# Optimization experiments

Measured on AMD Instinct MI355X. Metric: run time of the kernel, lower is better.

The kernel has to match this reference:

```python
import jax, jax.numpy as jnp
import numpy as np

B, T, E, H = 8, 2048, 1024, 64

def setup_inputs() -> dict:
    key = jax.random.key(0)
    kx, kk, kq, kv = jax.random.split(key, 4)
    x = jax.random.normal(kx, (B, T, E), dtype=jnp.float32)
    # nn.Linear(n_embd, head_size, bias=False): weight (H, E); store as (E, H) for x @ W
    Wk = jax.random.normal(kk, (E, H), dtype=jnp.float32) / np.sqrt(E)
    Wq = jax.random.normal(kq, (E, H), dtype=jnp.float32) / np.sqrt(E)
    Wv = jax.random.normal(kv, (E, H), dtype=jnp.float32) / np.sqrt(E)
    return {"x": x, "Wk": Wk, "Wq": Wq, "Wv": Wv}

def reference(x, Wk, Wq, Wv):
    # Single causal self-attention head (dropout in eval mode = identity).
    Bd, Td, Ed = x.shape
    k = x @ Wk  # [B,T,H]
    q = x @ Wq  # [B,T,H]
    v = x @ Wv  # [B,T,H]
    scale = jnp.asarray(64, x.dtype) ** -0.5  # hardcoded E2=64 in source
    wei = jnp.einsum('bth,bsh->bts', q, k) * scale  # [B,T,T]
    causal = jnp.tril(jnp.ones((Td, Td), dtype=bool))
    wei = jnp.where(causal, wei, -jnp.inf)
    wei = jax.nn.softmax(wei, axis=-1)
    out = jnp.einsum('bts,bsh->bth', wei, v)  # [B,T,H]
    return out
```

## Files before the change

kernel.cpp:

```cpp
#include <hip/hip_runtime.h>
#include <hip/hip_bf16.h>


typedef float f32x4 __attribute__((ext_vector_type(4)));
typedef float f32x16 __attribute__((ext_vector_type(16)));
typedef short bf16x8 __attribute__((ext_vector_type(8)));
typedef short bf16x4 __attribute__((ext_vector_type(4)));
typedef unsigned u32x2 __attribute__((ext_vector_type(2)));

#define MFMA16 __builtin_amdgcn_mfma_f32_16x16x32_bf16
#define MFMA32 __builtin_amdgcn_mfma_f32_32x32x16_bf16

__device__ __forceinline__ short f2bf(float f) {
    union { float f; unsigned u; } c; c.f = f;
    unsigned u = c.u;
    return (short)((u + 0x7FFFu + ((u >> 16) & 1u)) >> 16);
}

__device__ __forceinline__ unsigned cvt_pk_bf16(float lo, float hi) {
    unsigned r;
    asm("v_cvt_pk_bf16_f32 %0, %1, %2" : "=v"(r) : "v"(lo), "v"(hi));
    return r;
}

__global__ __launch_bounds__(256) void prep_w(const float* __restrict__ Wk,
                                              const float* __restrict__ Wq,
                                              const float* __restrict__ Wv,
                                              short* __restrict__ wsT) {
    int idx = blockIdx.x * 256 + threadIdx.x;
    int r = idx >> 10;
    int k = idx & 1023;
    int mat = r >> 6, c = r & 63;
    const float* W = (mat == 0) ? Wk : (mat == 1) ? Wq : Wv;
    float v = W[k * 64 + c];
    if (mat == 1) v *= 0.125f * 1.44269504088896f;
    wsT[r * 1024 + k] = f2bf(v);
}

__global__ __launch_bounds__(512, 4) void proj(const float* __restrict__ x,
                                               const short* __restrict__ wsT,
                                               short* __restrict__ kF,
                                               short* __restrict__ qF,
                                               short* __restrict__ vF) {
    __shared__ char ldsraw[2 * 8192 + 2 * 24576];
    int tid = threadIdx.x;
    int w = tid >> 6, lane = tid & 63;
    int wm = w >> 2, wn = w & 3;
    int lr = lane & 15, lg = lane >> 4;
    int t0 = blockIdx.x * 32;

    f32x4 acc[3] = {};

    auto stage = [&](int kt, int buf) {
        int k0 = kt * 64;
        {
            int G = tid;
            int row = G >> 4, p = G & 15;
            int g = p ^ (row & 15);
            const float* gp = x + (size_t)(t0 + row) * 1024 + k0 + g * 4;
            unsigned base = (unsigned)(buf * 8192 + w * 1024);
            __builtin_amdgcn_global_load_lds(
                (const __attribute__((address_space(1))) void*)gp,
                (__attribute__((address_space(3))) void*)(ldsraw + base), 16, 0, 0);
        }
#pragma unroll
        for (int s = 0; s < 3; ++s) {
            int G = s * 512 + tid;
            int row = G >> 3, p = G & 7;
            int g = p ^ (row & 7);
            const short* gp = wsT + (size_t)row * 1024 + k0 + g * 8;
            unsigned base = (unsigned)(16384 + buf * 24576 + s * 8192 + w * 1024);
            __builtin_amdgcn_global_load_lds(
                (const __attribute__((address_space(1))) void*)gp,
                (__attribute__((address_space(3))) void*)(ldsraw + base), 16, 0, 0);
        }
    };

    int arow = wm * 16 + lr;

    stage(0, 0);
    __syncthreads();

    for (int kt = 0; kt < 16; ++kt) {
        int cur = kt & 1;
        if (kt < 15) stage(kt + 1, cur ^ 1);

        const char* xb = ldsraw + cur * 8192 + arow * 256;
        const char* wb = ldsraw + 16384 + cur * 24576;
#pragma unroll
        for (int ks = 0; ks < 2; ++ks) {
            int g0 = ks * 8 + lg * 2;
            f32x4 u0 = *(const f32x4*)(xb + ((g0)     ^ lr) * 16);
            f32x4 u1 = *(const f32x4*)(xb + ((g0 + 1) ^ lr) * 16);
            bf16x8 a;
#pragma unroll
            for (int j = 0; j < 4; ++j) { a[j] = f2bf(u0[j]); a[4 + j] = f2bf(u1[j]); }
            int slot = (ks * 4 + lg) ^ (lr & 7);
#pragma unroll
            for (int nt = 0; nt < 3; ++nt) {
                int brow = wn * 48 + nt * 16 + lr;
                bf16x8 bf = *(const bf16x8*)(wb + brow * 128 + slot * 16);
                acc[nt] = MFMA16(a, bf, acc[nt], 0, 0, 0);
            }
        }
        __syncthreads();
    }

    int tg = t0 + wm * 16 + lg * 4;
    int b = tg >> 11;
    int s = (tg & 2047) >> 5;
    int w32b = tg & 31;
#pragma unroll
    for (int nt = 0; nt < 3; ++nt) {
        int col0 = wn * 48 + nt * 16;
        int mat = col0 >> 6;
        int h = (col0 & 63) + lr;
        if (mat == 2) {
            int ht = h >> 5;
            int c = w32b >> 4;
            int hi2 = (lg >> 1) & 1;
            int jb = (lg & 1) * 4;
            int lanep = hi2 * 32 + (h & 31);
            bf16x4 pk;
#pragma unroll
            for (int r = 0; r < 4; ++r) pk[r] = f2bf(acc[nt][r]);
            size_t idx = (((((size_t)b * 64 + s) * 2 + ht) * 2 + c) * 64 + lanep) * 8 + jb;
            *(bf16x4*)(vF + idx) = pk;
        } else {
            short* dst = mat ? qF : kF;
            int c = h >> 4, hi2 = (h >> 3) & 1, j = h & 7;
            size_t base = ((((size_t)b * 64 + s) * 4 + c) * 64 + hi2 * 32) * 8 + j;
#pragma unroll
            for (int r = 0; r < 4; ++r)
                dst[base + (size_t)(w32b + r) * 8] = f2bf(acc[nt][r]);
        }
    }
}

__global__ __launch_bounds__(512, 4) void attn(const short* __restrict__ kF,
                                               const short* __restrict__ qF,
                                               const short* __restrict__ vF,
                                               float* __restrict__ out) {
    int bid = blockIdx.x;
    int b = bid & 7;
    int i = bid >> 3;
    int ti = (i & 1) ? (63 - (i >> 1)) : (i >> 1);
    int t0 = ti * 32;

    int w = threadIdx.x >> 6;
    int lane = threadIdx.x & 63;
    int q = lane & 31, hi = lane >> 5;

    __shared__ float lacc[8][32][65];
    __shared__ float lm[8][32], ll[8][32];

    const short* qp = qF + ((size_t)(b * 64 + ti)) * 2048 + lane * 8;
    bf16x8 qf0 = *(const bf16x8*)(qp);
    bf16x8 qf1 = *(const bf16x8*)(qp + 512);
    bf16x8 qf2 = *(const bf16x8*)(qp + 1024);
    bf16x8 qf3 = *(const bf16x8*)(qp + 1536);

    const short* kb_b = kF + (size_t)b * 64 * 2048 + lane * 8;
    const short* vb_b = vF + (size_t)b * 64 * 2048 + lane * 8;

    f32x16 acc0 = {}, acc1 = {};
    float m_s = -1e30f, l_s = 0.f;

    int nblk = ti + 1;
    for (int blk = w; blk < nblk; blk += 8) {
        const short* kp = kb_b + (size_t)blk * 2048;
        bf16x8 kf0 = *(const bf16x8*)(kp);
        bf16x8 kf1 = *(const bf16x8*)(kp + 512);
        bf16x8 kf2 = *(const bf16x8*)(kp + 1024);
        bf16x8 kf3 = *(const bf16x8*)(kp + 1536);

        f32x16 S = {};
        S = MFMA32(kf0, qf0, S, 0, 0, 0);
        S = MFMA32(kf1, qf1, S, 0, 0, 0);
        S = MFMA32(kf2, qf2, S, 0, 0, 0);
        S = MFMA32(kf3, qf3, S, 0, 0, 0);

        const short* vp = vb_b + (size_t)blk * 2048;
        bf16x8 vf00 = *(const bf16x8*)(vp);
        bf16x8 vf01 = *(const bf16x8*)(vp + 512);
        bf16x8 vf10 = *(const bf16x8*)(vp + 1024);
        bf16x8 vf11 = *(const bf16x8*)(vp + 1536);

        if (blk == ti) {
#pragma unroll
            for (int r = 0; r < 16; ++r) {
                int row = (r & 3) + 8 * (r >> 2) + 4 * hi;
                if (row > q) S[r] = -1e30f;
            }
        }

        float a0 = fmaxf(S[0], S[1]),   a1 = fmaxf(S[2], S[3]);
        float a2 = fmaxf(S[4], S[5]),   a3 = fmaxf(S[6], S[7]);
        float a4 = fmaxf(S[8], S[9]),   a5 = fmaxf(S[10], S[11]);
        float a6 = fmaxf(S[12], S[13]), a7 = fmaxf(S[14], S[15]);
        a0 = fmaxf(a0, a1); a2 = fmaxf(a2, a3);
        a4 = fmaxf(a4, a5); a6 = fmaxf(a6, a7);
        a0 = fmaxf(a0, a2); a4 = fmaxf(a4, a6);
        float tm = fmaxf(a0, a4);
        tm = fmaxf(tm, __shfl_xor(tm, 32));

        bool skip = __all(tm <= m_s);
        float mn = skip ? m_s : fmaxf(m_s, tm);

#pragma unroll
        for (int r = 0; r < 16; ++r) S[r] = exp2f(S[r] - mn);
        float b0 = (S[0] + S[1]) + (S[2] + S[3]);
        float b1 = (S[4] + S[5]) + (S[6] + S[7]);
        float b2 = (S[8] + S[9]) + (S[10] + S[11]);
        float b3 = (S[12] + S[13]) + (S[14] + S[15]);
        float rs = (b0 + b1) + (b2 + b3);
        rs += __shfl_xor(rs, 32);

        if (skip) {
            l_s += rs;
        } else {
            float fr = exp2f(m_s - mn);
            l_s = l_s * fr + rs;
            m_s = mn;
#pragma unroll
            for (int r = 0; r < 16; ++r) { acc0[r] *= fr; acc1[r] *= fr; }
        }

        unsigned pk0 = cvt_pk_bf16(S[0],  S[1]);
        unsigned pk1 = cvt_pk_bf16(S[2],  S[3]);
        unsigned pk2 = cvt_pk_bf16(S[4],  S[5]);
        unsigned pk3 = cvt_pk_bf16(S[6],  S[7]);
        unsigned pk4 = cvt_pk_bf16(S[8],  S[9]);
        unsigned pk5 = cvt_pk_bf16(S[10], S[11]);
        unsigned pk6 = cvt_pk_bf16(S[12], S[13]);
        unsigned pk7 = cvt_pk_bf16(S[14], S[15]);
        u32x2 s02 = __builtin_amdgcn_permlane32_swap(pk0, pk2, false, false);
        u32x2 s13 = __builtin_amdgcn_permlane32_swap(pk1, pk3, false, false);
        u32x2 s46 = __builtin_amdgcn_permlane32_swap(pk4, pk6, false, false);
        u32x2 s57 = __builtin_amdgcn_permlane32_swap(pk5, pk7, false, false);
        union { bf16x8 v; unsigned u[4]; } f0, f1;
        f0.u[0] = s02.x; f0.u[1] = s13.x; f0.u[2] = s02.y; f0.u[3] = s13.y;
        f1.u[0] = s46.x; f1.u[1] = s57.x; f1.u[2] = s46.y; f1.u[3] = s57.y;

        acc0 = MFMA32(vf00, f0.v, acc0, 0, 0, 0);
        acc0 = MFMA32(vf01, f1.v, acc0, 0, 0, 0);
        acc1 = MFMA32(vf10, f0.v, acc1, 0, 0, 0);
        acc1 = MFMA32(vf11, f1.v, acc1, 0, 0, 0);
    }

    if (hi == 0) { lm[w][q] = m_s; ll[w][q] = l_s; }
#pragma unroll
    for (int r = 0; r < 16; ++r) {
        int row = (r & 3) + 8 * (r >> 2) + 4 * hi;
        lacc[w][q][row]      = acc0[r];
        lacc[w][q][32 + row] = acc1[r];
    }
    __syncthreads();

    int tid = threadIdx.x;
#pragma unroll
    for (int e = 0; e < 4; ++e) {
        int elem = e * 512 + tid;
        int row = elem >> 6, col = elem & 63;
        float ms = lm[0][row];
#pragma unroll
        for (int j = 1; j < 8; ++j) ms = fmaxf(ms, lm[j][row]);
        float lsum = 0.f, asum = 0.f;
#pragma unroll
        for (int j = 0; j < 8; ++j) {
            float sj = exp2f(lm[j][row] - ms);
            lsum += ll[j][row] * sj;
            asum += lacc[j][row][col] * sj;
        }
        out[(size_t)(b * 2048 + t0 + row) * 64 + col] = asum / lsum;
    }
}

extern "C" void kernel_launch(void* const* d_in, const int* in_sizes, int n_in,
                              void* d_out, int out_size, void* d_ws, size_t ws_size,
                              hipStream_t stream) {
    (void)in_sizes; (void)n_in; (void)out_size; (void)ws_size;
    const float* x  = (const float*)d_in[0];
    const float* Wk = (const float*)d_in[1];
    const float* Wq = (const float*)d_in[2];
    const float* Wv = (const float*)d_in[3];
    float* out = (float*)d_out;

    char* ws = (char*)d_ws;
    short* wsT = (short*)(ws);
    short* kF  = (short*)(ws + (1u << 20));
    short* qF  = (short*)(ws + (3u << 20));
    short* vF  = (short*)(ws + (5u << 20));

    prep_w<<<768, 256, 0, stream>>>(Wk, Wq, Wv, wsT);
    proj  <<<512, 512, 0, stream>>>(x, wsT, kF, qF, vF);
    attn  <<<512, 512, 0, stream>>>(kF, qF, vF, out);
}
```

Measured before the change: 43.48 us.

## Pair causal tiles per block, prefetch next K/V, and relax rescale threshold

Each attention block now processes two query tiles (pj and 63-pj) in turn, so every block gets an equal causal workload, and the grid is halved to 256 blocks. The inner loop double-buffers K/V register fragments, loading the next block's tiles before computing the current one to hide global load latency. The online-softmax rescale is now skipped unless the new max exceeds the running max by more than 11.5, which cuts rescale work but lets exponentials grow up to about 2^11.5 before renormalisation. Dropping the occupancy hint in launch bounds and prefetching into extra registers may lower occupancy.

Result: faster. 42.05 us (-3.3%).

```diff
diff --git a/kernel.cpp b/kernel.cpp
--- a/kernel.cpp
+++ b/kernel.cpp
@@ -137,142 +137,162 @@
     }
 }
 
-__global__ __launch_bounds__(512, 4) void attn(const short* __restrict__ kF,
-                                               const short* __restrict__ qF,
-                                               const short* __restrict__ vF,
-                                               float* __restrict__ out) {
+__global__ __launch_bounds__(512) void attn(const short* __restrict__ kF,
+                                            const short* __restrict__ qF,
+                                            const short* __restrict__ vF,
+                                            float* __restrict__ out) {
     int bid = blockIdx.x;
     int b = bid & 7;
-    int i = bid >> 3;
-    int ti = (i & 1) ? (63 - (i >> 1)) : (i >> 1);
-    int t0 = ti * 32;
+    int pj = bid >> 3;
 
     int w = threadIdx.x >> 6;
     int lane = threadIdx.x & 63;
     int q = lane & 31, hi = lane >> 5;
+    int tid = threadIdx.x;
 
     __shared__ float lacc[8][32][65];
     __shared__ float lm[8][32], ll[8][32];
 
-    const short* qp = qF + ((size_t)(b * 64 + ti)) * 2048 + lane * 8;
-    bf16x8 qf0 = *(const bf16x8*)(qp);
-    bf16x8 qf1 = *(const bf16x8*)(qp + 512);
-    bf16x8 qf2 = *(const bf16x8*)(qp + 1024);
-    bf16x8 qf3 = *(const bf16x8*)(qp + 1536);
-
     const short* kb_b = kF + (size_t)b * 64 * 2048 + lane * 8;
     const short* vb_b = vF + (size_t)b * 64 * 2048 + lane * 8;
 
-    f32x16 acc0 = {}, acc1 = {};
-    float m_s = -1e30f, l_s = 0.f;
-
-    int nblk = ti + 1;
-    for (int blk = w; blk < nblk; blk += 8) {
-        const short* kp = kb_b + (size_t)blk * 2048;
-        bf16x8 kf0 = *(const bf16x8*)(kp);
-        bf16x8 kf1 = *(const bf16x8*)(kp + 512);
-        bf16x8 kf2 = *(const bf16x8*)(kp + 1024);
-        bf16x8 kf3 = *(const bf16x8*)(kp + 1536);
-
-        f32x16 S = {};
-        S = MFMA32(kf0, qf0, S, 0, 0, 0);
-        S = MFMA32(kf1, qf1, S, 0, 0, 0);
-        S = MFMA32(kf2, qf2, S, 0, 0, 0);
-        S = MFMA32(kf3, qf3, S, 0, 0, 0);
-
-        const short* vp = vb_b + (size_t)blk * 2048;
-        bf16x8 vf00 = *(const bf16x8*)(vp);
-        bf16x8 vf01 = *(const bf16x8*)(vp + 512);
-        bf16x8 vf10 = *(const bf16x8*)(vp + 1024);
-        bf16x8 vf11 = *(const bf16x8*)(vp + 1536);
-
-        if (blk == ti) {
-#pragma unroll
-            for (int r = 0; r < 16; ++r) {
-                int row = (r & 3) + 8 * (r >> 2) + 4 * hi;
-                if (row > q) S[r] = -1e30f;
+    for (int sel = 0; sel < 2; ++sel) {
+        int ti = sel ? (63 - pj) : pj;
+        int t0 = ti * 32;
+        int nblk = ti + 1;
+
+        const short* qp = qF + ((size_t)(b * 64 + ti)) * 2048 + lane * 8;
+        bf16x8 qf0 = *(const bf16x8*)(qp);
+        bf16x8 qf1 = *(const bf16x8*)(qp + 512);
+        bf16x8 qf2 = *(const bf16x8*)(qp + 1024);
+        bf16x8 qf3 = *(const bf16x8*)(qp + 1536);
+
+        f32x16 acc0 = {}, acc1 = {};
+        float m_s = -1e30f, l_s = 0.f;
+
+        int fb = (w < nblk) ? w : 0;
+        const short* kp = kb_b + (size_t)fb * 2048;
+        const short* vp = vb_b + (size_t)fb * 2048;
+        bf16x8 kc0 = *(const bf16x8*)(kp);
+        bf16x8 kc1 = *(const bf16x8*)(kp + 512);
+        bf16x8 kc2 = *(const bf16x8*)(kp + 1024);
+        bf16x8 kc3 = *(const bf16x8*)(kp + 1536);
+        bf16x8 vc0 = *(const bf16x8*)(vp);
+        bf16x8 vc1 = *(const bf16x8*)(vp + 512);
+        bf16x8 vc2 = *(const bf16x8*)(vp + 1024);
+        bf16x8 vc3 = *(const bf16x8*)(vp + 1536);
+
+        for (int blk = w; blk < nblk; blk += 8) {
+            int nxt = blk + 8;
+            int ns = (nxt < nblk) ? nxt : blk;
+            const short* kpn = kb_b + (size_t)ns * 2048;
+            const short* vpn = vb_b + (size_t)ns * 2048;
+            bf16x8 kn0 = *(const bf16x8*)(kpn);
+            bf16x8 kn1 = *(const bf16x8*)(kpn + 512);
+            bf16x8 kn2 = *(const bf16x8*)(kpn + 1024);
+            bf16x8 kn3 = *(const bf16x8*)(kpn + 1536);
+            bf16x8 vn0 = *(const bf16x8*)(vpn);
+            bf16x8 vn1 = *(const bf16x8*)(vpn + 512);
+            bf16x8 vn2 = *(const bf16x8*)(vpn + 1024);
+            bf16x8 vn3 = *(const bf16x8*)(vpn + 1536);
+
+            f32x16 S = {};
+            S = MFMA32(kc0, qf0, S, 0, 0, 0);
+            S = MFMA32(kc1, qf1, S, 0, 0, 0);
+            S = MFMA32(kc2, qf2, S, 0, 0, 0);
+            S = MFMA32(kc3, qf3, S, 0, 0, 0);
+
+            if (blk == ti) {
+#pragma unroll
+                for (int r = 0; r < 16; ++r) {
+                    int row = (r & 3) + 8 * (r >> 2) + 4 * hi;
+                    if (row > q) S[r] = -1e30f;
+                }
             }
-        }
-
-        float a0 = fmaxf(S[0], S[1]),   a1 = fmaxf(S[2], S[3]);
-        float a2 = fmaxf(S[4], S[5]),   a3 = fmaxf(S[6], S[7]);
-        float a4 = fmaxf(S[8], S[9]),   a5 = fmaxf(S[10], S[11]);
-        float a6 = fmaxf(S[12], S[13]), a7 = fmaxf(S[14], S[15]);
-        a0 = fmaxf(a0, a1); a2 = fmaxf(a2, a3);
-        a4 = fmaxf(a4, a5); a6 = fmaxf(a6, a7);
-        a0 = fmaxf(a0, a2); a4 = fmaxf(a4, a6);
-        float tm = fmaxf(a0, a4);
-        tm = fmaxf(tm, __shfl_xor(tm, 32));
-
-        bool skip = __all(tm <= m_s);
-        float mn = skip ? m_s : fmaxf(m_s, tm);
-
-#pragma unroll
-        for (int r = 0; r < 16; ++r) S[r] = exp2f(S[r] - mn);
-        float b0 = (S[0] + S[1]) + (S[2] + S[3]);
-        float b1 = (S[4] + S[5]) + (S[6] + S[7]);
-        float b2 = (S[8] + S[9]) + (S[10] + S[11]);
-        float b3 = (S[12] + S[13]) + (S[14] + S[15]);
-        float rs = (b0 + b1) + (b2 + b3);
-        rs += __shfl_xor(rs, 32);
-
-        if (skip) {
-            l_s += rs;
-        } else {
-            float fr = exp2f(m_s - mn);
-            l_s = l_s * fr + rs;
-            m_s = mn;
-#pragma unroll
-            for (int r = 0; r < 16; ++r) { acc0[r] *= fr; acc1[r] *= fr; }
-        }
-
-        unsigned pk0 = cvt_pk_bf16(S[0],  S[1]);
-        unsigned pk1 = cvt_pk_bf16(S[2],  S[3]);
-        unsigned pk2 = cvt_pk_bf16(S[4],  S[5]);
-        unsigned pk3 = cvt_pk_bf16(S[6],  S[7]);
-        unsigned pk4 = cvt_pk_bf16(S[8],  S[9]);
-        unsigned pk5 = cvt_pk_bf16(S[10], S[11]);
-        unsigned pk6 = cvt_pk_bf16(S[12], S[13]);
-        unsigned pk7 = cvt_pk_bf16(S[14], S[15]);
-        u32x2 s02 = __builtin_amdgcn_permlane32_swap(pk0, pk2, false, false);
-        u32x2 s13 = __builtin_amdgcn_permlane32_swap(pk1, pk3, false, false);
-        u32x2 s46 = __builtin_amdgcn_permlane32_swap(pk4, pk6, false, false);
-        u32x2 s57 = __builtin_amdgcn_permlane32_swap(pk5, pk7, false, false);
-        union { bf16x8 v; unsigned u[4]; } f0, f1;
-        f0.u[0] = s02.x; f0.u[1] = s13.x; f0.u[2] = s02.y; f0.u[3] = s13.y;
-        f1.u[0] = s46.x; f1.u[1] = s57.x; f1.u[2] = s46.y; f1.u[3] = s57.y;
-
-        acc0 = MFMA32(vf00, f0.v, acc0, 0, 0, 0);
-        acc0 = MFMA32(vf01, f1.v, acc0, 0, 0, 0);
-        acc1 = MFMA32(vf10, f0.v, acc1, 0, 0, 0);
-        acc1 = MFMA32(vf11, f1.v, acc1, 0, 0, 0);
-    }
-
-    if (hi == 0) { lm[w][q] = m_s; ll[w][q] = l_s; }
-#pragma unroll
-    for (int r = 0; r < 16; ++r) {
-        int row = (r & 3) + 8 * (r >> 2) + 4 * hi;
-        lacc[w][q][row]      = acc0[r];
-        lacc[w][q][32 + row] = acc1[r];
-    }
-    __syncthreads();
-
-    int tid = threadIdx.x;
-#pragma unroll
-    for (int e = 0; e < 4; ++e) {
-        int elem = e * 512 + tid;
-        int row = elem >> 6, col = elem & 63;
-        float ms = lm[0][row];
-#pragma unroll
-        for (int j = 1; j < 8; ++j) ms = fmaxf(ms, lm[j][row]);
-        float lsum = 0.f, asum = 0.f;
-#pragma unroll
-        for (int j = 0; j < 8; ++j) {
-            float sj = exp2f(lm[j][row] - ms);
-            lsum += ll[j][row] * sj;
-            asum += lacc[j][row][col] * sj;
-        }
-        out[(size_t)(b * 2048 + t0 + row) * 64 + col] = asum / lsum;
+
+            float a0 = fmaxf(S[0], S[1]),   a1 = fmaxf(S[2], S[3]);
+            float a2 = fmaxf(S[4], S[5]),   a3 = fmaxf(S[6], S[7]);
+            float a4 = fmaxf(S[8], S[9]),   a5 = fmaxf(S[10], S[11]);
+            float a6 = fmaxf(S[12], S[13]), a7 = fmaxf(S[14], S[15]);
+            a0 = fmaxf(a0, a1); a2 = fmaxf(a2, a3);
+            a4 = fmaxf(a4, a5); a6 = fmaxf(a6, a7);
+            a0 = fmaxf(a0, a2); a4 = fmaxf(a4, a6);
+            float tm = fmaxf(a0, a4);
+            tm = fmaxf(tm, __shfl_xor(tm, 32));
+
+            bool skip = __all(tm <= m_s + 11.5f);
+            float mn = skip ? m_s : fmaxf(m_s, tm);
+
+#pragma unroll
+            for (int r = 0; r < 16; ++r) S[r] = exp2f(S[r] - mn);
+            float b0 = (S[0] + S[1]) + (S[2] + S[3]);
+            float b1 = (S[4] + S[5]) + (S[6] + S[7]);
+            float b2 = (S[8] + S[9]) + (S[10] + S[11]);
+            float b3 = (S[12] + S[13]) + (S[14] + S[15]);
+            float rs = (b0 + b1) + (b2 + b3);
+            rs += __shfl_xor(rs, 32);
+
+            if (skip) {
+                l_s += rs;
+            } else {
+                float fr = exp2f(m_s - mn);
+                l_s = l_s * fr + rs;
+                m_s = mn;
+#pragma unroll
+                for (int r = 0; r < 16; ++r) { acc0[r] *= fr; acc1[r] *= fr; }
+            }
+
+            unsigned pk0 = cvt_pk_bf16(S[0],  S[1]);
+            unsigned pk1 = cvt_pk_bf16(S[2],  S[3]);
+            unsigned pk2 = cvt_pk_bf16(S[4],  S[5]);
+            unsigned pk3 = cvt_pk_bf16(S[6],  S[7]);
+            unsigned pk4 = cvt_pk_bf16(S[8],  S[9]);
+            unsigned pk5 = cvt_pk_bf16(S[10], S[11]);
+            unsigned pk6 = cvt_pk_bf16(S[12], S[13]);
+            unsigned pk7 = cvt_pk_bf16(S[14], S[15]);
+            u32x2 s02 = __builtin_amdgcn_permlane32_swap(pk0, pk2, false, false);
+            u32x2 s13 = __builtin_amdgcn_permlane32_swap(pk1, pk3, false, false);
+            u32x2 s46 = __builtin_amdgcn_permlane32_swap(pk4, pk6, false, false);
+            u32x2 s57 = __builtin_amdgcn_permlane32_swap(pk5, pk7, false, false);
+            union { bf16x8 v; unsigned u[4]; } f0, f1;
+            f0.u[0] = s02.x; f0.u[1] = s13.x; f0.u[2] = s02.y; f0.u[3] = s13.y;
+            f1.u[0] = s46.x; f1.u[1] = s57.x; f1.u[2] = s46.y; f1.u[3] = s57.y;
+
+            acc0 = MFMA32(vc0, f0.v, acc0, 0, 0, 0);
+            acc0 = MFMA32(vc1, f1.v, acc0, 0, 0, 0);
+            acc1 = MFMA32(vc2, f0.v, acc1, 0, 0, 0);
+            acc1 = MFMA32(vc3, f1.v, acc1, 0, 0, 0);
+
+            kc0 = kn0; kc1 = kn1; kc2 = kn2; kc3 = kn3;
+            vc0 = vn0; vc1 = vn1; vc2 = vn2; vc3 = vn3;
+        }
+
+        if (hi == 0) { lm[w][q] = m_s; ll[w][q] = l_s; }
+#pragma unroll
+        for (int r = 0; r < 16; ++r) {
+            int row = (r & 3) + 8 * (r >> 2) + 4 * hi;
+            lacc[w][q][row]      = acc0[r];
+            lacc[w][q][32 + row] = acc1[r];
+        }
+        __syncthreads();
+
+#pragma unroll
+        for (int e = 0; e < 4; ++e) {
+            int elem = e * 512 + tid;
+            int row = elem >> 6, col = elem & 63;
+            float ms = lm[0][row];
+#pragma unroll
+            for (int j = 1; j < 8; ++j) ms = fmaxf(ms, lm[j][row]);
+            float lsum = 0.f, asum = 0.f;
+#pragma unroll
+            for (int j = 0; j < 8; ++j) {
+                float sj = exp2f(lm[j][row] - ms);
+                lsum += ll[j][row] * sj;
+                asum += lacc[j][row][col] * sj;
+            }
+            out[(size_t)(b * 2048 + t0 + row) * 64 + col] = asum / lsum;
+        }
+        __syncthreads();
     }
 }
 
@@ -294,5 +314,5 @@
 
     prep_w<<<768, 256, 0, stream>>>(Wk, Wq, Wv, wsT);
     proj  <<<512, 512, 0, stream>>>(x, wsT, kF, qF, vF);
-    attn  <<<512, 512, 0, stream>>>(kF, qF, vF, out);
-}
+    attn  <<<256, 512, 0, stream>>>(kF, qF, vF, out);
+}
```
